# Kernel tuning notes

Hardware: AMD Instinct MI355X
Metric: run time of the kernel (lower is better)

The kernel has to match this reference:

```python
import jax, jax.numpy as jnp
import numpy as np

D_MODEL = 1024
H = 16
D_K = D_MODEL // H


def setup_inputs() -> dict:
    key = jax.random.key(0)
    ks = jax.random.split(key, 12)
    B, S = 2, 2048
    scale = 1.0 / np.sqrt(D_MODEL)
    inp = {
        "q": jax.random.normal(ks[0], (B, S, D_MODEL), jnp.float32),
        "k": jax.random.normal(ks[1], (B, S, D_MODEL), jnp.float32),
        "v": jax.random.normal(ks[2], (B, S, D_MODEL), jnp.float32),
        "mask": jnp.ones((B, 1, S, S), jnp.int32),
        "w_q": jax.random.normal(ks[3], (D_MODEL, D_MODEL), jnp.float32) * scale,
        "b_q": jnp.zeros((D_MODEL,), jnp.float32),
        "w_k": jax.random.normal(ks[4], (D_MODEL, D_MODEL), jnp.float32) * scale,
        "b_k": jnp.zeros((D_MODEL,), jnp.float32),
        "w_v": jax.random.normal(ks[5], (D_MODEL, D_MODEL), jnp.float32) * scale,
        "b_v": jnp.zeros((D_MODEL,), jnp.float32),
        "w_o": jax.random.normal(ks[6], (D_MODEL, D_MODEL), jnp.float32) * scale,
        "b_o": jnp.zeros((D_MODEL,), jnp.float32),
    }
    return inp


def _split_heads(x):
    B, S, _ = x.shape
    return x.reshape(B, S, H, D_K).transpose(0, 2, 1, 3)  # [B,H,S,Dk]


def reference(q, k, v, mask, w_q, b_q, w_k, b_k, w_v, b_v, w_o, b_o):
    # Linear projections (torch Linear: x @ W^T + b)
    query = _split_heads(q @ w_q.T + b_q)
    key = _split_heads(k @ w_k.T + b_k)
    value = _split_heads(v @ w_v.T + b_v)

    # scaled dot-product attention: [B,H,S,S]
    scores = jnp.einsum("bhqd,bhkd->bhqk", query, key) / jnp.sqrt(
        jnp.asarray(D_K, query.dtype)
    )
    scores = jnp.where(mask == 0, jnp.asarray(-1e9, scores.dtype), scores)
    attn = jax.nn.softmax(scores, axis=-1)  # dropout p=0.0 -> identity
    out = jnp.einsum("bhqk,bhkd->bhqd", attn, value)  # [B,H,S,Dk]

    # combine heads -> [B,S,D_MODEL]
    B = out.shape[0]
    out = out.transpose(0, 2, 1, 3).reshape(B, -1, D_MODEL)
    return out @ w_o.T + b_o
```

## Files before the change

### kernel.cpp

```cpp
#include <hip/hip_runtime.h>
#include <hip/hip_bf16.h>

#define S_LEN 2048
#define BATCH 2
#define NH    16
#define DK    64
#define DM    1024

typedef __bf16 bf16x8 __attribute__((ext_vector_type(8)));
typedef float  f32x4  __attribute__((ext_vector_type(4)));
typedef ushort u16x8  __attribute__((ext_vector_type(8)));

__device__ __forceinline__ float bf2f(ushort u) {
    union { unsigned int i; float f; } v; v.i = ((unsigned int)u) << 16; return v.f;
}
__device__ __forceinline__ ushort f2bf(float f) {
    union { float f; unsigned int i; } v; v.f = f;
    unsigned int u = v.i;
    unsigned int r = u + 0x7fff + ((u >> 16) & 1);
    return (ushort)(r >> 16);
}

__device__ __forceinline__ void async_copy16(const ushort* g, ushort* l) {
    __builtin_amdgcn_global_load_lds(
        (__attribute__((address_space(1))) void*)(g),
        (__attribute__((address_space(3))) void*)(l), 16, 0, 0);
}

__global__ void detect(const ushort* __restrict__ q, int* __restrict__ flags) {
    __shared__ int red[256];
    int tid = threadIdx.x;
    int cnt = 0;
    for (int i = tid; i < 2048; i += 256) {
        ushort e = q[2 * i];
        int ex = (e >> 7) & 0xFF;
        if (ex == 0 || (ex >= 107 && ex <= 147)) cnt++;
    }
    red[tid] = cnt;
    __syncthreads();
    for (int s = 128; s > 0; s >>= 1) {
        if (tid < s) red[tid] += red[tid + s];
        __syncthreads();
    }
    if (tid == 0) {
        flags[0] = (red[0] < 1229) ? 1 : 0;
        flags[1] = 0;
    }
}

__global__ void mask_check(const int* __restrict__ mask, int* __restrict__ flags) {
    const int total = BATCH * S_LEN * S_LEN / 4;
    int idx = blockIdx.x * blockDim.x + threadIdx.x;
    int stride = gridDim.x * blockDim.x;
    bool bad = false;
    for (int i = idx; i < total; i += stride) {
        int4 v = ((const int4*)mask)[i];
        if (v.x == 0 || v.y == 0 || v.z == 0 || v.w == 0) bad = true;
    }
    if (__any(bad)) {
        if ((threadIdx.x & 63) == 0) atomicOr(&flags[1], 1);
    }
}

#define NJOBS 11
struct CvtJobs { const void* src[NJOBS]; };

__device__ __constant__ const int g_cum[NJOBS + 1] = {
    0, 4194304, 8388608, 12582912, 13631488, 14680064, 15728640,
    16777216, 16778240, 16779264, 16780288, 16781312
};

__global__ __launch_bounds__(256) void convert_all(CvtJobs J, ushort* __restrict__ conv,
                                                   const int* __restrict__ flags) {
    bool isf32 = flags[0] != 0;
    const int total_chunks = 16781312 / 8;
    int c = blockIdx.x * blockDim.x + threadIdx.x;
    int stride = gridDim.x * blockDim.x;
    for (; c < total_chunks; c += stride) {
        int e = c * 8;
        int j = 0;
        while (j + 1 < NJOBS + 1 && e >= g_cum[j + 1]) j++;
        int local = e - g_cum[j];
        if (isf32) {
            const float* s = (const float*)J.src[j] + local;
            f32x4 a = *(const f32x4*)s;
            f32x4 b = *(const f32x4*)(s + 4);
            ushort o[8] = { f2bf(a[0]), f2bf(a[1]), f2bf(a[2]), f2bf(a[3]),
                            f2bf(b[0]), f2bf(b[1]), f2bf(b[2]), f2bf(b[3]) };
            *(ushort4*)&conv[e]     = *(ushort4*)&o[0];
            *(ushort4*)&conv[e + 4] = *(ushort4*)&o[4];
        } else {
            const ushort* s = (const ushort*)J.src[j] + local;
            bf16x8 v = *(const bf16x8*)s;
            *(bf16x8*)&conv[e] = v;
        }
    }
}

struct GArg { const ushort* x; const ushort* w; const ushort* bias; void* y; int split; float scale; };

#define ASTR 40

__global__ __launch_bounds__(256) void gemm_bt(GArg a0, GArg a1, GArg a2,
                                               const int* __restrict__ flags) {
    GArg A = (blockIdx.z == 0) ? a0 : (blockIdx.z == 1 ? a1 : a2);
    const int K = 1024, N = 1024;
    __shared__ ushort As[128 * ASTR];
    __shared__ ushort Bs[128 * ASTR];

    int tid = threadIdx.x;
    int w = tid >> 6, lane = tid & 63;
    int wm = (w >> 1) * 64, wn = (w & 1) * 64;
    int m0 = blockIdx.y * 128, n0 = blockIdx.x * 128;

    f32x4 acc[4][4] = {};

    int row0 = tid >> 2;
    int pos  = (tid & 3) * 8;
    int row1 = row0 + 64;

    int fr = lane & 15;
    int qd = lane >> 4;

    const ushort* xp = A.x;
    const ushort* wp = A.w;

    for (int k0 = 0; k0 < K; k0 += 32) {
        bf16x8 ax0 = *(const bf16x8*)&xp[(size_t)(m0 + row0) * K + k0 + pos];
        bf16x8 ax1 = *(const bf16x8*)&xp[(size_t)(m0 + row1) * K + k0 + pos];
        bf16x8 bx0 = *(const bf16x8*)&wp[(size_t)(n0 + row0) * K + k0 + pos];
        bf16x8 bx1 = *(const bf16x8*)&wp[(size_t)(n0 + row1) * K + k0 + pos];
        __syncthreads();
        *(bf16x8*)&As[row0 * ASTR + pos] = ax0;
        *(bf16x8*)&As[row1 * ASTR + pos] = ax1;
        *(bf16x8*)&Bs[row0 * ASTR + pos] = bx0;
        *(bf16x8*)&Bs[row1 * ASTR + pos] = bx1;
        __syncthreads();

        bf16x8 af[4], bfr[4];
#pragma unroll
        for (int i = 0; i < 4; i++) {
            af[i]  = *(const bf16x8*)&As[(wm + i * 16 + fr) * ASTR + qd * 8];
            bfr[i] = *(const bf16x8*)&Bs[(wn + i * 16 + fr) * ASTR + qd * 8];
        }
#pragma unroll
        for (int i = 0; i < 4; i++)
#pragma unroll
            for (int j = 0; j < 4; j++)
                acc[i][j] = __builtin_amdgcn_mfma_f32_16x16x32_bf16(af[i], bfr[j], acc[i][j], 0, 0, 0);
    }

    bool isf32 = flags[0] != 0;
    int crow = qd * 4;
    int ccol = fr;
#pragma unroll
    for (int j = 0; j < 4; j++) {
        int n_g = n0 + wn + j * 16 + ccol;
        float bias = bf2f(A.bias[n_g]);
#pragma unroll
        for (int i = 0; i < 4; i++) {
#pragma unroll
            for (int r = 0; r < 4; r++) {
                int m_g = m0 + wm + i * 16 + crow + r;
                float val = (acc[i][j][r] + bias) * A.scale;
                if (A.split) {
                    int bb = m_g >> 11, s = m_g & 2047;
                    int h = n_g >> 6, d = n_g & 63;
                    ((ushort*)A.y)[((size_t)(bb * NH + h) * S_LEN + s) * DK + d] = f2bf(val);
                } else if (isf32) {
                    ((float*)A.y)[(size_t)m_g * N + n_g] = val;
                } else {
                    ((ushort*)A.y)[(size_t)m_g * N + n_g] = f2bf(val);
                }
            }
        }
    }
}

#define VSTR 72
#define PSTR 76

__global__ __launch_bounds__(256) void attn(const ushort* __restrict__ qp,
                                            const ushort* __restrict__ kp,
                                            const ushort* __restrict__ vp,
                                            const int* __restrict__ mask,
                                            const int* __restrict__ flags,
                                            ushort* __restrict__ ctx) {
    __shared__ ushort Ks[64 * 64];
    __shared__ ushort Vt[64 * VSTR];
    __shared__ ushort Pb[4][32 * PSTR];

    int tid = threadIdx.x, w = tid >> 6, lane = tid & 63;
    int bh = blockIdx.y;
    int b = bh >> 4, h = bh & 15;
    int q0 = blockIdx.x * 128;

    const ushort* qb = qp + (size_t)bh * S_LEN * DK;
    const ushort* kb = kp + (size_t)bh * S_LEN * DK;
    const ushort* vb = vp + (size_t)bh * S_LEN * DK;
    const int* mb = mask + (size_t)b * S_LEN * S_LEN;
    bool do_mask = flags[1] != 0;

    int fr = lane & 15;
    int qd = lane >> 4;

    bf16x8 qf[2][2];
#pragma unroll
    for (int rt = 0; rt < 2; rt++)
#pragma unroll
        for (int kc = 0; kc < 2; kc++)
            qf[rt][kc] = *(const bf16x8*)&qb[(size_t)(q0 + w * 32 + rt * 16 + fr) * DK + kc * 32 + qd * 8];

    bf16x8 ones;
#pragma unroll
    for (int j = 0; j < 8; j++) ones[j] = (__bf16)1.0f;

    f32x4 oacc[2][4] = {};
    f32x4 lacc[2] = {};

    int kschunk = ((lane & 7) ^ ((lane >> 3) & 7)) * 8;
    int ksrow0 = w * 8 + (lane >> 3);
    int ksrow1 = (w + 4) * 8 + (lane >> 3);
    int vc0 = w * 8, vc1 = (w + 4) * 8;

    for (int k0 = 0; k0 < S_LEN; k0 += 64) {
        u16x8 vx0 = *(const u16x8*)&vb[(size_t)(k0 + lane) * DK + vc0];
        u16x8 vx1 = *(const u16x8*)&vb[(size_t)(k0 + lane) * DK + vc1];
        __syncthreads();
        async_copy16(&kb[(size_t)(k0 + ksrow0) * DK + kschunk], &Ks[w * 512]);
        async_copy16(&kb[(size_t)(k0 + ksrow1) * DK + kschunk], &Ks[(w + 4) * 512]);
#pragma unroll
        for (int j = 0; j < 8; j++) {
            Vt[(vc0 + j) * VSTR + lane] = vx0[j];
            Vt[(vc1 + j) * VSTR + lane] = vx1[j];
        }
        __syncthreads();

        f32x4 sc[2][4] = {};
#pragma unroll
        for (int kc = 0; kc < 2; kc++) {
            bf16x8 kf[4];
#pragma unroll
            for (int ct = 0; ct < 4; ct++) {
                int key = ct * 16 + fr;
                kf[ct] = *(const bf16x8*)&Ks[key * 64 + (((kc * 4 + qd) ^ (fr & 7)) * 8)];
            }
#pragma unroll
            for (int rt = 0; rt < 2; rt++)
#pragma unroll
                for (int ct = 0; ct < 4; ct++)
                    sc[rt][ct] = __builtin_amdgcn_mfma_f32_16x16x32_bf16(qf[rt][kc], kf[ct], sc[rt][ct], 0, 0, 0);
        }

        if (do_mask) {
#pragma unroll
            for (int rt = 0; rt < 2; rt++)
#pragma unroll
                for (int ct = 0; ct < 4; ct++)
#pragma unroll
                    for (int r = 0; r < 4; r++) {
                        int qr = q0 + w * 32 + rt * 16 + qd * 4 + r;
                        int kcid = k0 + ct * 16 + fr;
                        if (mb[(size_t)qr * S_LEN + kcid] == 0) sc[rt][ct][r] = -1e9f;
                    }
        }

#pragma unroll
        for (int rt = 0; rt < 2; rt++)
#pragma unroll
            for (int ct = 0; ct < 4; ct++)
#pragma unroll
                for (int r = 0; r < 4; r++) {
                    union { float f; ushort2 hh; } t;
                    t.f = __builtin_amdgcn_exp2f(sc[rt][ct][r]);
                    Pb[w][(rt * 16 + qd * 4 + r) * PSTR + ct * 16 + fr] = t.hh.y;
                }

#pragma unroll
        for (int kk = 0; kk < 2; kk++) {
            bf16x8 pf[2], vf[4];
#pragma unroll
            for (int rt = 0; rt < 2; rt++)
                pf[rt] = *(const bf16x8*)&Pb[w][(rt * 16 + fr) * PSTR + kk * 32 + qd * 8];
#pragma unroll
            for (int dt = 0; dt < 4; dt++)
                vf[dt] = *(const bf16x8*)&Vt[(dt * 16 + fr) * VSTR + kk * 32 + qd * 8];
#pragma unroll
            for (int rt = 0; rt < 2; rt++) {
                lacc[rt] = __builtin_amdgcn_mfma_f32_16x16x32_bf16(pf[rt], ones, lacc[rt], 0, 0, 0);
#pragma unroll
                for (int dt = 0; dt < 4; dt++)
                    oacc[rt][dt] = __builtin_amdgcn_mfma_f32_16x16x32_bf16(pf[rt], vf[dt], oacc[rt][dt], 0, 0, 0);
            }
        }
    }

#pragma unroll
    for (int rt = 0; rt < 2; rt++)
#pragma unroll
        for (int r = 0; r < 4; r++) {
            float inv = 1.0f / lacc[rt][r];
            int qr = q0 + w * 32 + rt * 16 + qd * 4 + r;
            size_t rowbase = ((size_t)(b * S_LEN + qr) * NH + h) * DK;
#pragma unroll
            for (int dt = 0; dt < 4; dt++)
                ctx[rowbase + dt * 16 + fr] = f2bf(oacc[rt][dt][r] * inv);
        }
}

extern "C" void kernel_launch(void* const* d_in, const int* in_sizes, int n_in,
                              void* d_out, int out_size, void* d_ws, size_t ws_size,
                              hipStream_t stream) {
    const int* mask = (const int*)d_in[3];

    char* ws = (char*)d_ws;
    int*    flags = (int*)ws;
    ushort* conv  = (ushort*)(ws + 4096);
    const size_t conv_bytes = 16781312ull * 2;
    char* p = ws + 4096 + ((conv_bytes + 4095) & ~4095ull);
    size_t sz = (size_t)BATCH * NH * S_LEN * DK * sizeof(ushort);
    ushort* qp  = (ushort*)(p);
    ushort* kp  = (ushort*)(p + sz);
    ushort* vp  = (ushort*)(p + 2 * sz);
    ushort* ctx = (ushort*)(p + 3 * sz);

    ushort* qc  = conv + 0;
    ushort* kc  = conv + 4194304;
    ushort* vc  = conv + 8388608;
    ushort* wqc = conv + 12582912;
    ushort* wkc = conv + 13631488;
    ushort* wvc = conv + 14680064;
    ushort* woc = conv + 15728640;
    ushort* bqc = conv + 16777216;
    ushort* bkc = conv + 16778240;
    ushort* bvc = conv + 16779264;
    ushort* boc = conv + 16780288;

    detect<<<1, 256, 0, stream>>>((const ushort*)d_in[0], flags);
    mask_check<<<1024, 256, 0, stream>>>(mask, flags);

    CvtJobs J;
    J.src[0] = d_in[0];  J.src[1] = d_in[1];  J.src[2] = d_in[2];
    J.src[3] = d_in[4];  J.src[4] = d_in[6];  J.src[5] = d_in[8];
    J.src[6] = d_in[10]; J.src[7] = d_in[5];  J.src[8] = d_in[7];
    J.src[9] = d_in[9];  J.src[10] = d_in[11];
    convert_all<<<2048, 256, 0, stream>>>(J, conv, flags);

    const float cs = 0.125f * 1.44269504f;
    GArg aq{qc, wqc, bqc, qp, 1, cs};
    GArg ak{kc, wkc, bkc, kp, 1, 1.0f};
    GArg av{vc, wvc, bvc, vp, 1, 1.0f};
    gemm_bt<<<dim3(8, 32, 3), 256, 0, stream>>>(aq, ak, av, flags);

    attn<<<dim3(16, 32), 256, 0, stream>>>(qp, kp, vp, mask, flags, ctx);

    GArg ao{ctx, woc, boc, d_out, 0, 1.0f};
    gemm_bt<<<dim3(8, 32, 1), 256, 0, stream>>>(ao, ao, ao, flags);
}
```

Measured before the change: 300.9 us.

## Double-buffer GEMM tiles with async LDS loads, swizzle, and remap block order

The projection GEMM now stages its A and B tiles with asynchronous global-to-LDS copies into two LDS buffers. The next K slice is fetched while MFMAs run on the current one, which also removes one barrier per iteration. LDS padding is replaced by an XOR swizzle on the 8-element chunk index to avoid bank conflicts. Both the GEMM and the attention kernel remap the linear block id to change tile traversal order for cache locality. Correctness depends on the async copies being complete before the barrier is reached.

```diff
diff --git a/kernel.cpp b/kernel.cpp
--- a/kernel.cpp
+++ b/kernel.cpp
@@ -99,50 +99,60 @@
 
 struct GArg { const ushort* x; const ushort* w; const ushort* bias; void* y; int split; float scale; };
 
-#define ASTR 40
-
 __global__ __launch_bounds__(256) void gemm_bt(GArg a0, GArg a1, GArg a2,
                                                const int* __restrict__ flags) {
     GArg A = (blockIdx.z == 0) ? a0 : (blockIdx.z == 1 ? a1 : a2);
     const int K = 1024, N = 1024;
-    __shared__ ushort As[128 * ASTR];
-    __shared__ ushort Bs[128 * ASTR];
+    __shared__ ushort As[2][128 * 32];
+    __shared__ ushort Bs[2][128 * 32];
 
     int tid = threadIdx.x;
     int w = tid >> 6, lane = tid & 63;
     int wm = (w >> 1) * 64, wn = (w & 1) * 64;
-    int m0 = blockIdx.y * 128, n0 = blockIdx.x * 128;
+
+    int id = blockIdx.x + 8 * blockIdx.y;
+    int m0 = (id & 31) * 128;
+    int n0 = (id >> 5) * 128;
 
     f32x4 acc[4][4] = {};
 
-    int row0 = tid >> 2;
-    int pos  = (tid & 3) * 8;
-    int row1 = row0 + 64;
+    int srow0 = w * 16 + (lane >> 2);
+    int srow1 = (w + 4) * 16 + (lane >> 2);
+    int schunk = ((lane & 3) ^ ((lane >> 3) & 3)) * 8;
 
     int fr = lane & 15;
     int qd = lane >> 4;
-
-    const ushort* xp = A.x;
-    const ushort* wp = A.w;
-
-    for (int k0 = 0; k0 < K; k0 += 32) {
-        bf16x8 ax0 = *(const bf16x8*)&xp[(size_t)(m0 + row0) * K + k0 + pos];
-        bf16x8 ax1 = *(const bf16x8*)&xp[(size_t)(m0 + row1) * K + k0 + pos];
-        bf16x8 bx0 = *(const bf16x8*)&wp[(size_t)(n0 + row0) * K + k0 + pos];
-        bf16x8 bx1 = *(const bf16x8*)&wp[(size_t)(n0 + row1) * K + k0 + pos];
+    int fcp = (qd ^ ((fr >> 1) & 3)) * 8;
+
+    const ushort* xr0 = A.x + (size_t)(m0 + srow0) * K + schunk;
+    const ushort* xr1 = A.x + (size_t)(m0 + srow1) * K + schunk;
+    const ushort* wr0 = A.w + (size_t)(n0 + srow0) * K + schunk;
+    const ushort* wr1 = A.w + (size_t)(n0 + srow1) * K + schunk;
+
+    async_copy16(xr0, &As[0][w * 512]);
+    async_copy16(xr1, &As[0][(w + 4) * 512]);
+    async_copy16(wr0, &Bs[0][w * 512]);
+    async_copy16(wr1, &Bs[0][(w + 4) * 512]);
+
+    for (int k = 0; k < 32; k++) {
         __syncthreads();
-        *(bf16x8*)&As[row0 * ASTR + pos] = ax0;
-        *(bf16x8*)&As[row1 * ASTR + pos] = ax1;
-        *(bf16x8*)&Bs[row0 * ASTR + pos] = bx0;
-        *(bf16x8*)&Bs[row1 * ASTR + pos] = bx1;
-        __syncthreads();
+        int cur = k & 1, nxt = cur ^ 1;
 
         bf16x8 af[4], bfr[4];
 #pragma unroll
         for (int i = 0; i < 4; i++) {
-            af[i]  = *(const bf16x8*)&As[(wm + i * 16 + fr) * ASTR + qd * 8];
-            bfr[i] = *(const bf16x8*)&Bs[(wn + i * 16 + fr) * ASTR + qd * 8];
-        }
+            af[i]  = *(const bf16x8*)&As[cur][(wm + i * 16 + fr) * 32 + fcp];
+            bfr[i] = *(const bf16x8*)&Bs[cur][(wn + i * 16 + fr) * 32 + fcp];
+        }
+
+        if (k + 1 < 32) {
+            int off = (k + 1) * 32;
+            async_copy16(xr0 + off, &As[nxt][w * 512]);
+            async_copy16(xr1 + off, &As[nxt][(w + 4) * 512]);
+            async_copy16(wr0 + off, &Bs[nxt][w * 512]);
+            async_copy16(wr1 + off, &Bs[nxt][(w + 4) * 512]);
+        }
+
 #pragma unroll
         for (int i = 0; i < 4; i++)
 #pragma unroll
@@ -191,9 +201,10 @@
     __shared__ ushort Pb[4][32 * PSTR];
 
     int tid = threadIdx.x, w = tid >> 6, lane = tid & 63;
-    int bh = blockIdx.y;
+    int id = blockIdx.x + 16 * blockIdx.y;
+    int bh = id & 31;
     int b = bh >> 4, h = bh & 15;
-    int q0 = blockIdx.x * 128;
+    int q0 = (id >> 5) * 128;
 
     const ushort* qb = qp + (size_t)bh * S_LEN * DK;
     const ushort* kb = kp + (size_t)bh * S_LEN * DK;
```

After: 284.2 us. 5.6% less time.
